# Performance work log

Hardware: AMD Instinct MI355X
Metric: run time of the kernel (lower is better)

The kernel has to match this reference:

```python
import jax, jax.numpy as jnp
from jax import lax
import numpy as np

KSIZE = 3      # match-patch size
STRIDE = 1
RATE = 2       # down/up-sampling rate
FUSE_K = 3
SCALE = 10.0   # softmax scale
DN = ('NHWC', 'HWIO', 'NHWC')


def extract_patches(x, k, s):
    """tf.image.extract_patches(..., padding='SAME'); returns [B, L, k, k, C]."""
    B, H, W, C = x.shape
    oh, ow = -(-H // s), -(-W // s)
    ph = max((oh - 1) * s + k - H, 0)
    pw = max((ow - 1) * s + k - W, 0)
    xp = jnp.pad(x, ((0, 0), (ph // 2, ph - ph // 2), (pw // 2, pw - pw // 2), (0, 0)))
    cols = [xp[:, i:i + oh * s:s, j:j + ow * s:s, :] for i in range(k) for j in range(k)]
    p = jnp.stack(cols, axis=3)                 # [B, oh, ow, k*k, C]
    return p.reshape(B, oh * ow, k, k, C)


def setup_inputs() -> dict:
    key = jax.random.key(0)
    k1, k2, k3 = jax.random.split(key, 3)
    B, H, W, C = 4, 96, 96, 64
    f = jax.random.normal(k1, (B, H, W, C), jnp.float32)
    b = jax.random.normal(k2, (B, H, W, C), jnp.float32)
    mask = jnp.zeros((B, H, W, 1), jnp.float32)          # 0 = no hole -> all patches valid
    fuse_weight = jax.random.normal(k3, (FUSE_K, FUSE_K, 1, 1), jnp.float32) * 0.3
    return {"f": f, "b": b, "mask": mask, "fuse_weight": fuse_weight}


def reference(f, b, mask, fuse_weight):
    B, H, W, C = f.shape
    kernel = 2 * RATE
    # deconv kernels from full-res background: [B, 4, 4, C, L]
    raw_w = extract_patches(b, kernel, RATE * STRIDE).transpose(0, 2, 3, 4, 1)
    fd = f[:, 1::2, 1::2, :]
    bd = b[:, 1::2, 1::2, :]
    md = mask[:, 1::2, 1::2, :]
    h, w_ = fd.shape[1], fd.shape[2]
    L = h * w_
    # matching kernels from downscaled background: [B, 3, 3, C, L]
    wk = extract_patches(bd, KSIZE, STRIDE).transpose(0, 2, 3, 4, 1)
    # mask patches -> per-patch validity mm: [B, L]
    mp = extract_patches(md, KSIZE, STRIDE)
    mm = (jnp.mean(mp, axis=(2, 3, 4)) == 0.0).astype(f.dtype)

    def per_sample(xi, wi, rwi, mmi):
        # xi: [h, w, C]; wi: [3,3,C,L]; rwi: [4,4,C,L]; mmi: [L]
        norm = jnp.maximum(jnp.sqrt(jnp.sum(wi * wi, axis=(0, 1, 2))), 1e-4)
        yi = lax.conv_general_dilated(xi[None], wi / norm, (1, 1), 'SAME',
                                      dimension_numbers=DN)[0]        # [h, w, L]
        # fuse: 3x3 conv over flattened [HW, HW] score map, twice (transposed view)
        y = yi.reshape(1, L, L, 1)
        y = lax.conv_general_dilated(y, fuse_weight, (1, 1), 'SAME', dimension_numbers=DN)
        y = y.reshape(h, w_, h, w_).transpose(1, 0, 3, 2).reshape(1, L, L, 1)
        y = lax.conv_general_dilated(y, fuse_weight, (1, 1), 'SAME', dimension_numbers=DN)
        y = y.reshape(w_, h, w_, h).transpose(1, 0, 3, 2).reshape(h, w_, L)
        # mask-gated scaled softmax over background patches
        y = y * mmi
        y = jax.nn.softmax(y * SCALE, axis=-1) * mmi
        # deconv-style combine with raw 4x4 patches, stride=rate
        out = lax.conv_transpose(y[None], rwi, (RATE, RATE), 'SAME',
                                 dimension_numbers=DN, transpose_kernel=True)[0] / 4.0
        return out                                                    # [H, W, C]

    return jax.vmap(per_sample)(fd, wk, raw_w, mm)
```

## Files before the change

### kernel.cpp

```cpp
#include <hip/hip_runtime.h>
#include <hip/hip_bf16.h>

#define KL  2304
#define KC  64
#define KHS 48
#define KHH 96
#define OFFY (KHS*(KL + 1))

typedef __attribute__((ext_vector_type(8))) short bf16x8;
typedef __attribute__((ext_vector_type(4))) short bf16x4;
typedef __attribute__((ext_vector_type(8))) _Float16 f16x8;
typedef __attribute__((ext_vector_type(4))) _Float16 f16x4;
typedef __attribute__((ext_vector_type(4))) float f32x4;

static __device__ inline unsigned short f2bf(float x) {
    __hip_bfloat16 h = __float2bfloat16(x);
    return *reinterpret_cast<unsigned short*>(&h);
}
static __device__ inline float bf2f(unsigned short u) {
    unsigned v = ((unsigned)u) << 16;
    return __uint_as_float(v);
}
static __device__ inline unsigned short f2h(float x) {
    _Float16 h = (_Float16)x;
    return *reinterpret_cast<unsigned short*>(&h);
}
static __device__ inline float h2f(unsigned short u) {
    _Float16 h = *reinterpret_cast<_Float16*>(&u);
    return (float)h;
}

__global__ __launch_bounds__(256) void k_prep2(const float* __restrict__ f,
    const float* __restrict__ bsrc, const float* __restrict__ mask,
    float* __restrict__ nbuf, float* __restrict__ mdd,
    unsigned short* __restrict__ Ahat, unsigned short* __restrict__ Bhat)
{
    int pp = blockIdx.x*4 + (threadIdx.x >> 6);
    int c = threadIdx.x & 63;
    int p = pp % KL, bi = pp / KL;
    int y = p / KHS, x = p % KHS;
    int fy = 2*y + 1;
    unsigned short* Ap = Ahat + ((size_t)bi*KL + p)*192;
    unsigned short* Bp = Bhat + ((size_t)bi*KL + p)*192;
    float bc = 0.f;
    #pragma unroll
    for (int dxi = 0; dxi < 3; dxi++) {
        int xx = x + dxi - 1;
        float av = 0.f, bv = 0.f;
        if ((unsigned)xx < KHS) {
            int fxx = 2*xx + 1;
            size_t src = (((size_t)bi*KHH + fy)*KHH + fxx)*KC + c;
            av = f[src]; bv = bsrc[src];
        }
        if (dxi == 1) bc = bv;
        Ap[dxi*64 + c] = f2h(av);
        Bp[dxi*64 + c] = f2h(bv);
    }
    float s = bc*bc;
    #pragma unroll
    for (int off = 32; off > 0; off >>= 1) s += __shfl_down(s, off);
    if (c == 0) {
        nbuf[bi*KL + p] = s;
        mdd[bi*KL + p]  = mask[((size_t)bi*KHH + fy)*KHH + (2*x + 1)];
    }
}

__global__ __launch_bounds__(256) void k_normmask(const float* __restrict__ nbuf,
    const float* __restrict__ mdd, float* __restrict__ rnrm, float* __restrict__ mm)
{
    int i = blockIdx.x*256 + threadIdx.x;
    int q = i % KL, bi = i / KL;
    int v = q / KHS, u = q % KHS;
    float sn = 0.f, sm = 0.f;
    for (int dy = -1; dy <= 1; dy++) {
        int vv = v + dy; if ((unsigned)vv >= KHS) continue;
        for (int dx = -1; dx <= 1; dx++) {
            int uu = u + dx; if ((unsigned)uu >= KHS) continue;
            sn += nbuf[bi*KL + vv*KHS + uu];
            sm += mdd[bi*KL + vv*KHS + uu];
        }
    }
    rnrm[i] = 1.0f / fmaxf(sqrtf(sn), 1e-4f);
    mm[i]   = (sm == 0.0f) ? 1.0f : 0.0f;
}

template<int KITERS, int OUTMODE, bool INFP16>
__global__ __launch_bounds__(256) void k_mfma_bt(const unsigned short* __restrict__ A,
    const unsigned short* __restrict__ B, void* __restrict__ Cv,
    int Ncols, size_t sA, size_t sB, size_t sC, int KDIM, int nsplit, size_t psize)
{
    int flat = blockIdx.x + gridDim.x*(blockIdx.y + gridDim.y*blockIdx.z);
    int nxy = gridDim.x*gridDim.y;
    int per = (nxy*gridDim.z) >> 3;
    int g = (flat & 7)*per + (flat >> 3);
    int z = g / nxy; int r = g - z*nxy;
    int by = r / gridDim.x; int bx = r - by*gridDim.x;

    int ks = z % nsplit, bi = z / nsplit;
    int kbase = ks * KITERS * 32;
    int n0 = bx*128, m0 = by*128;
    const unsigned short* Ab = A + (size_t)bi*sA;
    const unsigned short* Bb = B + (size_t)bi*sB;
    __shared__ unsigned short As[128*32];
    __shared__ unsigned short Bs[128*32];
    int t = threadIdx.x;
    int lane = t & 63, w = t >> 6;
    int l15 = lane & 15, quad = lane >> 4;
    int swf = (l15 >> 2) & 3;
    int wm = (w >> 1)*64, wn = (w & 1)*64;
    int srow = lane >> 2;
    int ch = lane & 3;
    f32x4 acc[4][4];
    #pragma unroll
    for (int i = 0; i < 4; i++)
        #pragma unroll
        for (int j = 0; j < 4; j++) acc[i][j] = (f32x4){0.f,0.f,0.f,0.f};

    for (int kk = 0; kk < KITERS; kk++) {
        int k0 = kbase + kk*32;
        #pragma unroll
        for (int i = 0; i < 2; i++) {
            int rbase = w*32 + i*16;
            int r2 = rbase + srow;
            int cs = (ch ^ ((r2 >> 2) & 3))*8;
            const unsigned short* ga = &Ab[(size_t)(m0 + r2)*KDIM + k0 + cs];
            __builtin_amdgcn_global_load_lds(
                (const __attribute__((address_space(1))) void*)ga,
                (__attribute__((address_space(3))) void*)&As[rbase*32], 16, 0, 0);
            const unsigned short* gb = &Bb[(size_t)(n0 + r2)*KDIM + k0 + cs];
            __builtin_amdgcn_global_load_lds(
                (const __attribute__((address_space(1))) void*)gb,
                (__attribute__((address_space(3))) void*)&Bs[rbase*32], 16, 0, 0);
        }
        __syncthreads();
        if (INFP16) {
            f16x8 af[4], bfr[4];
            #pragma unroll
            for (int mi = 0; mi < 4; mi++)
                af[mi] = *(const f16x8*)&As[(wm + mi*16 + l15)*32 + ((quad ^ swf)*8)];
            #pragma unroll
            for (int ni = 0; ni < 4; ni++)
                bfr[ni] = *(const f16x8*)&Bs[(wn + ni*16 + l15)*32 + ((quad ^ swf)*8)];
            #pragma unroll
            for (int mi = 0; mi < 4; mi++)
                #pragma unroll
                for (int ni = 0; ni < 4; ni++)
                    acc[mi][ni] = __builtin_amdgcn_mfma_f32_16x16x32_f16(
                        af[mi], bfr[ni], acc[mi][ni], 0, 0, 0);
        } else {
            bf16x8 af[4], bfr[4];
            #pragma unroll
            for (int mi = 0; mi < 4; mi++)
                af[mi] = *(const bf16x8*)&As[(wm + mi*16 + l15)*32 + ((quad ^ swf)*8)];
            #pragma unroll
            for (int ni = 0; ni < 4; ni++)
                bfr[ni] = *(const bf16x8*)&Bs[(wn + ni*16 + l15)*32 + ((quad ^ swf)*8)];
            #pragma unroll
            for (int mi = 0; mi < 4; mi++)
                #pragma unroll
                for (int ni = 0; ni < 4; ni++)
                    acc[mi][ni] = __builtin_amdgcn_mfma_f32_16x16x32_bf16(
                        af[mi], bfr[ni], acc[mi][ni], 0, 0, 0);
        }
        __syncthreads();
    }
    if (OUTMODE == 1 || OUTMODE == 2) {
        unsigned short* Cb = (unsigned short*)Cv + (size_t)ks*psize + (size_t)bi*sC;
        #pragma unroll
        for (int mi = 0; mi < 4; mi++)
            #pragma unroll
            for (int ni = 0; ni < 4; ni++) {
                int col = n0 + wn + ni*16 + l15;
                #pragma unroll
                for (int r2 = 0; r2 < 4; r2++) {
                    int row = m0 + wm + mi*16 + quad*4 + r2;
                    Cb[(size_t)row*Ncols + col] = (OUTMODE == 1)
                        ? f2bf(acc[mi][ni][r2]) : f2h(acc[mi][ni][r2]);
                }
            }
    } else {
        float* Cb = (float*)Cv + (size_t)ks*psize + (size_t)bi*sC;
        #pragma unroll
        for (int mi = 0; mi < 4; mi++)
            #pragma unroll
            for (int ni = 0; ni < 4; ni++) {
                int col = n0 + wn + ni*16 + l15;
                #pragma unroll
                for (int r2 = 0; r2 < 4; r2++) {
                    int row = m0 + wm + mi*16 + quad*4 + r2;
                    Cb[(size_t)row*Ncols + col] = acc[mi][ni][r2];
                }
            }
    }
}

#define KP_NT 24
#define STGA4(tt, j) do {                                                      \
    __builtin_amdgcn_global_load_lds(                                          \
        (const __attribute__((address_space(1))) void*)(gA + (size_t)(j)*128*2304 + (size_t)(tt)*32), \
        (__attribute__((address_space(3))) void*)&Atile[(tt)&3][((j)*128 + (w<<4))*32], 16, 0, 0); \
} while (0)
#define STGB4(tt, j) do {                                                      \
    __builtin_amdgcn_global_load_lds(                                          \
        (const __attribute__((address_space(1))) void*)(gB + (size_t)(j)*128*2304 + (size_t)(tt)*32), \
        (__attribute__((address_space(3))) void*)&Btile[(tt)&3][((j)*128 + (w<<4))*32], 16, 0, 0); \
} while (0)

#define MFMA_B(a, b, c) __builtin_amdgcn_mfma_f32_16x16x32_bf16(a, b, c, 0, 0, 0)

#define KT_BODY(kt, BVU, BVF) do {                                             \
    const unsigned short* At = &Atile[(kt) & 3][0];                            \
                                                          \
    __builtin_amdgcn_s_barrier();                                              \
    _Pragma("unroll")                                                          \
    for (int i = 0; i < 4; i++)                                                \
        af1[i] = *(const bf16x8*)&At[aOff + 2048 + i*512];                     \
    if ((kt) + 3 < KP_NT) { STGA4((kt)+3, 0); STGA4((kt)+3, 1); }              \
    __builtin_amdgcn_s_setprio(1);                                             \
    _Pragma("unroll")                                                          \
    for (int mi = 0; mi < 4; mi++)                                             \
        _Pragma("unroll")                                                      \
        for (int ni = 0; ni < 4; ni++)                                         \
            acc[mi][ni] = MFMA_B(af0[mi], BVU[ni], acc[mi][ni]);               \
    __builtin_amdgcn_s_setprio(0);                                             \
                                                          \
    __builtin_amdgcn_s_barrier();                                              \
    if ((kt) < KP_NT-1) {                                                      \
        if ((kt) <= KP_NT-4)      asm volatile("s_waitcnt vmcnt(6)" ::: "memory"); \
        else if ((kt) == KP_NT-3) asm volatile("s_waitcnt vmcnt(4)" ::: "memory"); \
        else                      asm volatile("s_waitcnt vmcnt(0)" ::: "memory"); \
        __builtin_amdgcn_sched_barrier(0);                                     \
        const unsigned short* An = &Atile[((kt)+1) & 3][0];                    \
        const unsigned short* Bn = &Btile[((kt)+1) & 3][0];                    \
        _Pragma("unroll")                                                      \
        for (int i = 0; i < 4; i++)                                            \
            af0[i] = *(const bf16x8*)&An[aOff + i*512];                        \
        _Pragma("unroll")                                                      \
        for (int ni = 0; ni < 4; ni++)                                         \
            BVF[ni] = *(const bf16x8*)&Bn[bOff + ni*512];                      \
    }                                                                          \
    if ((kt) + 3 < KP_NT) { STGB4((kt)+3, 0); STGB4((kt)+3, 1); }              \
    __builtin_amdgcn_s_setprio(1);                                             \
    _Pragma("unroll")                                                          \
    for (int mi = 0; mi < 4; mi++)                                             \
        _Pragma("unroll")                                                      \
        for (int ni = 0; ni < 4; ni++)                                         \
            acc[4+mi][ni] = MFMA_B(af1[mi], BVU[ni], acc[4+mi][ni]);           \
    __builtin_amdgcn_s_setprio(0);                                             \
} while (0)

__global__ __launch_bounds__(512, 2) void k_p8(
    const unsigned short* __restrict__ A,
    const unsigned short* __restrict__ B,
    unsigned short* __restrict__ C,
    size_t psize)
{
    __shared__ unsigned short Atile[4][8192];
    __shared__ unsigned short Btile[4][8192];

    int flat = blockIdx.x + gridDim.x*(blockIdx.y + gridDim.y*blockIdx.z);
    int nwg = gridDim.x*gridDim.y*gridDim.z;
    int qq = nwg >> 3, rr8 = nwg & 7;
    int xcd = flat & 7, sub = flat >> 3;
    int g = (xcd < rr8 ? xcd*(qq+1) : rr8*(qq+1) + (xcd - rr8)*qq) + sub;
    int nxy = gridDim.x*gridDim.y;
    int z = g / nxy; int rg = g - z*nxy;
    int by = rg / gridDim.x; int bx = rg - by*gridDim.x;

    int ks = z % 3, bi = z / 3;
    int kbase = ks * 768;
    int m0 = by * 256, n0 = bx * 256;
    const unsigned short* Ab = A + (size_t)bi * (2304ull*2304);
    const unsigned short* Bb = B + (size_t)bi * (1024ull*2304);

    int t = threadIdx.x;
    int w = t >> 6, lane = t & 63;
    int wr = w >> 2, wc = w & 3;
    int l15 = lane & 15, quad = lane >> 4;

    int scol = ((t & 3) ^ ((t >> 3) & 3))*8;
    const unsigned short* gA = Ab + (size_t)(m0 + (t >> 2))*2304 + kbase + scol;
    const unsigned short* gB = Bb + (size_t)(n0 + (t >> 2))*2304 + kbase + scol;

    int csw = (quad ^ ((l15 >> 1) & 3))*8;
    int aOff = (wr*128 + l15)*32 + csw;
    int bOff = (wc*64  + l15)*32 + csw;

    f32x4 acc[8][4];
    #pragma unroll
    for (int mi = 0; mi < 8; mi++)
        #pragma unroll
        for (int ni = 0; ni < 4; ni++) acc[mi][ni] = (f32x4){0.f,0.f,0.f,0.f};

    #pragma unroll
    for (int tt = 0; tt < 3; tt++) {
        STGA4(tt, 0); STGA4(tt, 1);
        STGB4(tt, 0); STGB4(tt, 1);
    }
    asm volatile("s_waitcnt vmcnt(8)" ::: "memory");
    __builtin_amdgcn_s_barrier();

    bf16x8 af0[4], af1[4], bvA[4], bvB[4];
    #pragma unroll
    for (int i = 0; i < 4; i++)
        af0[i] = *(const bf16x8*)&Atile[0][aOff + i*512];
    #pragma unroll
    for (int ni = 0; ni < 4; ni++)
        bvA[ni] = *(const bf16x8*)&Btile[0][bOff + ni*512];

    #pragma unroll 1
    for (int ktp = 0; ktp < KP_NT/2; ktp++) {
        int kt0 = ktp*2;
        KT_BODY(kt0,     bvA, bvB);
        KT_BODY(kt0 + 1, bvB, bvA);
    }

    unsigned short* Cb = C + (size_t)ks*psize + (size_t)bi*(2304ull*1024);
    #pragma unroll
    for (int mi = 0; mi < 8; mi++)
        #pragma unroll
        for (int ni = 0; ni < 4; ni++) {
            int col = n0 + wc*64 + ni*16 + l15;
            int rowb = m0 + wr*128 + mi*16 + quad*4;
            #pragma unroll
            for (int r = 0; r < 4; r++)
                Cb[(size_t)(rowb + r)*1024 + col] = f2bf(acc[mi][ni][r]);
        }
}

__global__ __launch_bounds__(256) void k_fuse_a2(const unsigned short* __restrict__ T,
    const float* __restrict__ rnrm, const float* __restrict__ fw,
    unsigned short* __restrict__ Y1)
{
    __shared__ float Sl[10][280];
    int flat = blockIdx.x + 9*(blockIdx.y + 288*blockIdx.z);
    int nwg = 2592*gridDim.z;
    int cpx = nwg >> 3;
    int g = (flat & 7)*cpx + (flat >> 3);
    int bi = g / 2592; int rem = g - bi*2592;
    int by = rem / 9;  int qt = rem - by*9;

    int p0 = by*8, q0 = qt*256;
    const unsigned short* Tb = T + (size_t)bi*KL*KL;
    const float* rn = rnrm + bi*KL;
    int t = threadIdx.x;
    bool edge = (qt == 0) | (qt == 8);
    if (!edge) {
        for (int idx = t; idx < 10*34; idx += 256) {
            int r = idx / 34, j = idx - r*34;
            int pp = p0 - 1 + r;
            int qq0 = q0 - 8 + j*8;
            float s[8];
            #pragma unroll
            for (int k = 0; k < 8; k++) s[k] = 0.f;
            if ((unsigned)pp < KL) {
                size_t base = (size_t)pp*KL + qq0;
                bool bm = (pp >= KHS), bp = (pp < KL - KHS);
                size_t offm = bm ? (size_t)OFFY : 0;
                size_t offp = bp ? (size_t)OFFY : 0;
                float fm = bm ? 1.f : 0.f, fp2 = bp ? 1.f : 0.f;
                f16x8 v0 = *(const f16x8*)&Tb[base];
                f16x8 vm = *(const f16x8*)&Tb[base - offm];
                f16x8 vp = *(const f16x8*)&Tb[base + offp];
                #pragma unroll
                for (int k = 0; k < 8; k++)
                    s[k] = ((float)v0[k] + fm*(float)vm[k] + fp2*(float)vp[k]) * rn[qq0 + k];
            }
            #pragma unroll
            for (int k = 0; k < 8; k++) Sl[r][j*8 + k] = s[k];
        }
    } else {
        for (int idx = t; idx < 10*272; idx += 256) {
            int r = idx / 272, c = idx - r*272;
            int pp = p0 - 1 + r, qq = q0 - 8 + c;
            float s = 0.f;
            if ((unsigned)pp < KL && (unsigned)qq < KL) {
                size_t base = (size_t)pp*KL + qq;
                float acc = h2f(Tb[base]);
                if (pp >= KHS && qq >= KHS)         acc += h2f(Tb[base - OFFY]);
                if (pp < KL - KHS && qq < KL - KHS) acc += h2f(Tb[base + OFFY]);
                s = acc * rn[qq];
            }
            Sl[r][c] = s;
        }
    }
    __syncthreads();
    float w[9];
    #pragma unroll
    for (int i = 0; i < 9; i++) w[i] = fw[i];
    int q = q0 + t;
    float h0[10], h1[10], h2[10];
    #pragma unroll
    for (int r = 0; r < 10; r++) {
        float s0 = Sl[r][t+7], s1 = Sl[r][t+8], s2 = Sl[r][t+9];
        h0[r] = w[0]*s0 + w[1]*s1 + w[2]*s2;
        h1[r] = w[3]*s0 + w[4]*s1 + w[5]*s2;
        h2[r] = w[6]*s0 + w[7]*s1 + w[8]*s2;
    }
    #pragma unroll
    for (int rr = 0; rr < 8; rr++) {
        Y1[((size_t)bi*KL + p0 + rr)*KL + q] = f2h(h0[rr] + h1[rr+1] + h2[rr+2]);
    }
}

__global__ __launch_bounds__(256) void k_fuse_b(const unsigned short* __restrict__ Y1,
    const float* __restrict__ fw, const float* __restrict__ mm,
    unsigned short* __restrict__ Ybf)
{
    __shared__ float rowb[6][KL];
    int blk = blockIdx.x;
    int tp0 = (blk % 576)*4;
    int bi  = blk / 576;
    int t = threadIdx.x;
    const unsigned short* Yb = Y1 + (size_t)bi*KL*KL;
    for (int idx = t; idx < 6*(KL/8); idx += 256) {
        int a = idx / (KL/8), i = idx - a*(KL/8);
        int t2 = tp0 - 1 + a;
        if ((unsigned)t2 < KL) {
            int pr = (t2 % KHS)*KHS + t2/KHS;
            f16x8 v = *(const f16x8*)&Yb[(size_t)pr*KL + i*8];
            #pragma unroll
            for (int j = 0; j < 8; j++) rowb[a][i*8 + j] = (float)v[j];
        } else {
            #pragma unroll
            for (int j = 0; j < 8; j++) rowb[a][i*8 + j] = 0.f;
        }
    }
    float w9[9];
    #pragma unroll
    for (int i = 0; i < 9; i++) w9[i] = fw[i];
    __syncthreads();
    int w = t >> 6, lane = t & 63;
    int tp = tp0 + w;
    int x = tp / KHS, y = tp - x*KHS;
    int p = y*KHS + x;
    const float* mmb = mm + bi*KL;
    float vals[36];
    float lmax = -1e30f;
    #pragma unroll
    for (int i = 0; i < 36; i++) {
        int q = lane + i*64;
        int qm = (q >= KHS)      ? q - KHS : 2255 + q;
        int qp = (q <= KL-1-KHS) ? q + KHS : q - 2255;
        float fm = (q != 0)    ? 1.f : 0.f;
        float fp = (q != KL-1) ? 1.f : 0.f;
        float am = w9[0]*rowb[w][qm] + w9[3]*rowb[w+1][qm] + w9[6]*rowb[w+2][qm];
        float a0 = w9[1]*rowb[w][q]  + w9[4]*rowb[w+1][q]  + w9[7]*rowb[w+2][q];
        float ap = w9[2]*rowb[w][qp] + w9[5]*rowb[w+1][qp] + w9[8]*rowb[w+2][qp];
        float val = (fm*am + a0 + fp*ap) * mmb[q] * 10.0f;
        vals[i] = val;
        lmax = fmaxf(lmax, val);
    }
    #pragma unroll
    for (int off = 32; off > 0; off >>= 1) lmax = fmaxf(lmax, __shfl_down(lmax, off));
    lmax = __shfl(lmax, 0);
    float lsum = 0.f;
    #pragma unroll
    for (int i = 0; i < 36; i++) {
        float e = __expf(vals[i] - lmax);
        vals[i] = e;
        lsum += e;
    }
    #pragma unroll
    for (int off = 32; off > 0; off >>= 1) lsum += __shfl_down(lsum, off);
    lsum = __shfl(lsum, 0);
    float inv = 1.0f / lsum;
    unsigned short* orow = Ybf + ((size_t)bi*KL + p)*KL;
    #pragma unroll
    for (int i = 0; i < 36; i++) {
        int q = lane + i*64;
        orow[q] = f2bf(vals[i]*inv*mmb[q]);
    }
}

__global__ __launch_bounds__(256) void k_buildRt(const float* __restrict__ bsrc,
    unsigned short* __restrict__ Rt)
{
    __shared__ unsigned short Ls[2][48][65];
    int blk = blockIdx.x;
    int vb = blk % 24;
    int jj = (blk / 24) % 16;
    int bi = blk / 384;
    int ky = jj >> 2, kx = jj & 3;
    int v0 = vb*2;
    int t = threadIdx.x;
    int c = t & 63, u4 = t >> 6;

    #pragma unroll
    for (int vv = 0; vv < 2; vv++) {
        int ry = 2*(v0 + vv) + ky - 1;
        bool ryok = (unsigned)ry < KHH;
        const float* brow = bsrc + (((size_t)bi*KHH + (ryok ? ry : 0))*KHH)*KC;
        #pragma unroll
        for (int j = 0; j < 12; j++) {
            int u = u4*12 + j;
            int rx = 2*u + kx - 1;
            float val = 0.f;
            if (ryok && (unsigned)rx < KHH)
                val = brow[(size_t)rx*KC + c];
            Ls[vv][u][c] = f2bf(val);
        }
    }
    __syncthreads();

    int cn = t >> 2, part = t & 3;
    unsigned short* orow = Rt + ((size_t)bi*1024 + jj*64 + cn)*KL + vb*96;
    #pragma unroll
    for (int ch = 0; ch < 3; ch++) {
        int ql = part*24 + ch*8;
        int vv = ql / 48;
        int ub = ql - vv*48;
        bf16x8 v8;
        #pragma unroll
        for (int j = 0; j < 8; j++)
            v8[j] = (short)Ls[vv][ub + j][cn];
        *(bf16x8*)&orow[ql] = v8;
    }
}

__global__ __launch_bounds__(256) void k_overlap(const unsigned short* __restrict__ P,
    float* __restrict__ out, size_t psize)
{
    size_t gid = (size_t)blockIdx.x*256 + threadIdx.x;
    int c8 = (int)(gid & 7)*8;
    size_t r = gid >> 3;
    int ix = (int)(r % KHH); r /= KHH;
    int iy = (int)(r % KHH);
    int bi = (int)(r / KHH);
    float acc[8];
    #pragma unroll
    for (int j = 0; j < 8; j++) acc[j] = 0.f;
    #pragma unroll
    for (int sy = 0; sy < 2; sy++) {
        int ky = (iy & 1) ? (sy*2) : (sy*2 + 1);
        int yp = (iy + 1 - ky) >> 1;
        if ((unsigned)yp >= KHS) continue;
        #pragma unroll
        for (int sx = 0; sx < 2; sx++) {
            int kx = (ix & 1) ? (sx*2) : (sx*2 + 1);
            int xp = (ix + 1 - kx) >> 1;
            if ((unsigned)xp >= KHS) continue;
            size_t idx = (((size_t)bi*KL + yp*KHS + xp)*16 + (ky*4 + kx))*64 + c8;
            #pragma unroll
            for (int s = 0; s < 3; s++) {
                bf16x8 v = *(const bf16x8*)&P[idx + s*psize];
                #pragma unroll
                for (int j = 0; j < 8; j++)
                    acc[j] += bf2f((unsigned short)v[j]);
            }
        }
    }
    float* op = &out[(((size_t)bi*KHH + iy)*KHH + ix)*KC + c8];
    f32x4 o0 = (f32x4){acc[0], acc[1], acc[2], acc[3]} * 0.25f;
    f32x4 o1 = (f32x4){acc[4], acc[5], acc[6], acc[7]} * 0.25f;
    *(f32x4*)&op[0] = o0;
    *(f32x4*)&op[4] = o1;
}

extern "C" void kernel_launch(void* const* d_in, const int* in_sizes, int n_in,
                              void* d_out, int out_size, void* d_ws, size_t ws_size,
                              hipStream_t stream)
{
    const float* f    = (const float*)d_in[0];
    const float* b    = (const float*)d_in[1];
    const float* mask = (const float*)d_in[2];
    const float* fw   = (const float*)d_in[3];
    float* out = (float*)d_out;

    auto need = [](int nbc) -> size_t {
        return (size_t)nbc * (2ull*KL*KC + 4ull*KL + 2ull*(size_t)KL*KL) * 4ull;
    };
    int nbc = 4;
    if (need(nbc) > ws_size) nbc = 2;
    if (need(nbc) > ws_size) nbc = 1;

    for (int bi0 = 0; bi0 < 4; bi0 += nbc) {
        int nb = (4 - bi0 < nbc) ? (4 - bi0) : nbc;
        const float* fc = f    + (size_t)bi0*KHH*KHH*KC;
        const float* bc = b    + (size_t)bi0*KHH*KHH*KC;
        const float* mc = mask + (size_t)bi0*KHH*KHH;
        float* outc = out + (size_t)bi0*KHH*KHH*KC;

        float* w    = (float*)d_ws;
        float* nbuf = w;  w += (size_t)nbc*KL;
        float* mdd  = w;  w += (size_t)nbc*KL;
        float* rnrm = w;  w += (size_t)nbc*KL;
        float* mmb  = w;  w += (size_t)nbc*KL;
        float* bufA = w;  w += (size_t)nbc*KL*KL;
        float* bufB = w;
        unsigned short* Ahat = (unsigned short*)bufB;
        unsigned short* Bhat = Ahat + (size_t)nbc*KL*192;
        unsigned short* Tbuf = (unsigned short*)bufA;
        unsigned short* Y1   = (unsigned short*)bufB;
        unsigned short* Ybf = (unsigned short*)bufA;
        unsigned short* Rtb = Ybf + (size_t)nbc*KL*KL;
        unsigned short* Pbuf = (unsigned short*)bufB;
        size_t psize = (size_t)nbc*KL*1024;

        k_prep2     <<<nb*KL/4, 256, 0, stream>>>(fc, bc, mc, nbuf, mdd, Ahat, Bhat);
        k_normmask  <<<(nb*KL)/256, 256, 0, stream>>>(nbuf, mdd, rnrm, mmb);
        k_mfma_bt<6,2,true><<<dim3(18, 18, nb), 256, 0, stream>>>(
            Ahat, Bhat, Tbuf, KL, (size_t)KL*192, (size_t)KL*192, (size_t)KL*KL,
            192, 1, 0);
        k_fuse_a2   <<<dim3(9, 288, nb), 256, 0, stream>>>(Tbuf, rnrm, fw, Y1);
        k_fuse_b    <<<nb*576, 256, 0, stream>>>(Y1, fw, mmb, Ybf);
        k_buildRt   <<<nb*384, 256, 0, stream>>>(bc, Rtb);
        k_p8<<<dim3(4, 9, nb*3), 512, 0, stream>>>(Ybf, Rtb, Pbuf, psize);
        k_overlap   <<<nb*288, 256, 0, stream>>>(Pbuf, outc, psize);
    }
}
```

Baseline: 242.5 us.

## Replace generic score GEMM with 256x256-tile pipelined fp16 MFMA kernel

The first matching GEMM (patch features times background patches, K=192) moves from the generic 128x128 single-buffered kernel to a dedicated 512-thread kernel with 256x256 tiles. It uses a 4-stage LDS ring with asynchronous global-to-LDS loads issued three tiles ahead, explicit vmcnt waits, raw barriers and setprio around the MFMA bursts. The aim is to overlap loads with MFMA work and increase reuse per tile. The costs are higher LDS and register use per block, and a smaller grid (324 blocks) that may leave some CUs idle.

```diff
diff --git a/kernel.cpp b/kernel.cpp
--- a/kernel.cpp
+++ b/kernel.cpp
@@ -84,114 +84,135 @@
     mm[i]   = (sm == 0.0f) ? 1.0f : 0.0f;
 }
 
-template<int KITERS, int OUTMODE, bool INFP16>
-__global__ __launch_bounds__(256) void k_mfma_bt(const unsigned short* __restrict__ A,
-    const unsigned short* __restrict__ B, void* __restrict__ Cv,
-    int Ncols, size_t sA, size_t sB, size_t sC, int KDIM, int nsplit, size_t psize)
-{
+#define TP_NT 6
+#define T_STGA(tt, j) do {                                                     \
+    __builtin_amdgcn_global_load_lds(                                          \
+        (const __attribute__((address_space(1))) void*)(gA + (size_t)(j)*128*192 + (size_t)(tt)*32), \
+        (__attribute__((address_space(3))) void*)&Atile[(tt)&3][((j)*128 + (w<<4))*32], 16, 0, 0); \
+} while (0)
+#define T_STGB(tt, j) do {                                                     \
+    __builtin_amdgcn_global_load_lds(                                          \
+        (const __attribute__((address_space(1))) void*)(gB + (size_t)(j)*128*192 + (size_t)(tt)*32), \
+        (__attribute__((address_space(3))) void*)&Btile[(tt)&3][((j)*128 + (w<<4))*32], 16, 0, 0); \
+} while (0)
+
+#define MFMA_H(a, b, c) __builtin_amdgcn_mfma_f32_16x16x32_f16(a, b, c, 0, 0, 0)
+
+#define KT_BODY_T(kt, BVU, BVF) do {                                           \
+    const unsigned short* At = &Atile[(kt) & 3][0];                            \
+                                                          \
+    __builtin_amdgcn_s_barrier();                                              \
+    _Pragma("unroll")                                                          \
+    for (int i = 0; i < 4; i++)                                                \
+        af1[i] = *(const f16x8*)&At[aOff + 2048 + i*512];                      \
+    if ((kt) + 3 < TP_NT) { T_STGA((kt)+3, 0); T_STGA((kt)+3, 1); }            \
+    __builtin_amdgcn_s_setprio(1);                                             \
+    _Pragma("unroll")                                                          \
+    for (int mi = 0; mi < 4; mi++)                                             \
+        _Pragma("unroll")                                                      \
+        for (int ni = 0; ni < 4; ni++)                                         \
+            acc[mi][ni] = MFMA_H(af0[mi], BVU[ni], acc[mi][ni]);               \
+    __builtin_amdgcn_s_setprio(0);                                             \
+                                                          \
+    __builtin_amdgcn_s_barrier();                                              \
+    if ((kt) < TP_NT-1) {                                                      \
+        if ((kt) <= TP_NT-4)      asm volatile("s_waitcnt vmcnt(6)" ::: "memory"); \
+        else if ((kt) == TP_NT-3) asm volatile("s_waitcnt vmcnt(4)" ::: "memory"); \
+        else                      asm volatile("s_waitcnt vmcnt(0)" ::: "memory"); \
+        __builtin_amdgcn_sched_barrier(0);                                     \
+        const unsigned short* An = &Atile[((kt)+1) & 3][0];                    \
+        const unsigned short* Bn = &Btile[((kt)+1) & 3][0];                    \
+        _Pragma("unroll")                                                      \
+        for (int i = 0; i < 4; i++)                                            \
+            af0[i] = *(const f16x8*)&An[aOff + i*512];                         \
+        _Pragma("unroll")                                                      \
+        for (int ni = 0; ni < 4; ni++)                                         \
+            BVF[ni] = *(const f16x8*)&Bn[bOff + ni*512];                       \
+    }                                                                          \
+    if ((kt) + 3 < TP_NT) { T_STGB((kt)+3, 0); T_STGB((kt)+3, 1); }            \
+    __builtin_amdgcn_s_setprio(1);                                             \
+    _Pragma("unroll")                                                          \
+    for (int mi = 0; mi < 4; mi++)                                             \
+        _Pragma("unroll")                                                      \
+        for (int ni = 0; ni < 4; ni++)                                         \
+            acc[4+mi][ni] = MFMA_H(af1[mi], BVU[ni], acc[4+mi][ni]);           \
+    __builtin_amdgcn_s_setprio(0);                                             \
+} while (0)
+
+__global__ __launch_bounds__(512, 2) void k_t8(
+    const unsigned short* __restrict__ A,
+    const unsigned short* __restrict__ B,
+    unsigned short* __restrict__ T)
+{
+    __shared__ unsigned short Atile[4][8192];
+    __shared__ unsigned short Btile[4][8192];
+
     int flat = blockIdx.x + gridDim.x*(blockIdx.y + gridDim.y*blockIdx.z);
+    int nwg = gridDim.x*gridDim.y*gridDim.z;
+    int qq = nwg >> 3, rr8 = nwg & 7;
+    int xcd = flat & 7, sub = flat >> 3;
+    int g = (xcd < rr8 ? xcd*(qq+1) : rr8*(qq+1) + (xcd - rr8)*qq) + sub;
     int nxy = gridDim.x*gridDim.y;
-    int per = (nxy*gridDim.z) >> 3;
-    int g = (flat & 7)*per + (flat >> 3);
-    int z = g / nxy; int r = g - z*nxy;
-    int by = r / gridDim.x; int bx = r - by*gridDim.x;
-
-    int ks = z % nsplit, bi = z / nsplit;
-    int kbase = ks * KITERS * 32;
-    int n0 = bx*128, m0 = by*128;
-    const unsigned short* Ab = A + (size_t)bi*sA;
-    const unsigned short* Bb = B + (size_t)bi*sB;
-    __shared__ unsigned short As[128*32];
-    __shared__ unsigned short Bs[128*32];
+    int bi = g / nxy; int rg = g - bi*nxy;
+    int by = rg / gridDim.x; int bx = rg - by*gridDim.x;
+
+    int m0 = by * 256, n0 = bx * 256;
+    const unsigned short* Ab = A + (size_t)bi * ((size_t)KL*192);
+    const unsigned short* Bb = B + (size_t)bi * ((size_t)KL*192);
+
     int t = threadIdx.x;
-    int lane = t & 63, w = t >> 6;
+    int w = t >> 6, lane = t & 63;
+    int wr = w >> 2, wc = w & 3;
     int l15 = lane & 15, quad = lane >> 4;
-    int swf = (l15 >> 2) & 3;
-    int wm = (w >> 1)*64, wn = (w & 1)*64;
-    int srow = lane >> 2;
-    int ch = lane & 3;
-    f32x4 acc[4][4];
+
+    int scol = ((t & 3) ^ ((t >> 3) & 3))*8;
+    const unsigned short* gA = Ab + (size_t)(m0 + (t >> 2))*192 + scol;
+    const unsigned short* gB = Bb + (size_t)(n0 + (t >> 2))*192 + scol;
+
+    int csw = (quad ^ ((l15 >> 1) & 3))*8;
+    int aOff = (wr*128 + l15)*32 + csw;
+    int bOff = (wc*64  + l15)*32 + csw;
+
+    f32x4 acc[8][4];
+    #pragma unroll
+    for (int mi = 0; mi < 8; mi++)
+        #pragma unroll
+        for (int ni = 0; ni < 4; ni++) acc[mi][ni] = (f32x4){0.f,0.f,0.f,0.f};
+
+    #pragma unroll
+    for (int tt = 0; tt < 3; tt++) {
+        T_STGA(tt, 0); T_STGA(tt, 1);
+        T_STGB(tt, 0); T_STGB(tt, 1);
+    }
+    asm volatile("s_waitcnt vmcnt(8)" ::: "memory");
+    __builtin_amdgcn_s_barrier();
+
+    f16x8 af0[4], af1[4], bvA[4], bvB[4];
     #pragma unroll
     for (int i = 0; i < 4; i++)
+        af0[i] = *(const f16x8*)&Atile[0][aOff + i*512];
+    #pragma unroll
+    for (int ni = 0; ni < 4; ni++)
+        bvA[ni] = *(const f16x8*)&Btile[0][bOff + ni*512];
+
+    #pragma unroll 1
+    for (int ktp = 0; ktp < TP_NT/2; ktp++) {
+        int kt0 = ktp*2;
+        KT_BODY_T(kt0,     bvA, bvB);
+        KT_BODY_T(kt0 + 1, bvB, bvA);
+    }
+
+    unsigned short* Tb = T + (size_t)bi*((size_t)KL*KL);
+    #pragma unroll
+    for (int mi = 0; mi < 8; mi++)
         #pragma unroll
-        for (int j = 0; j < 4; j++) acc[i][j] = (f32x4){0.f,0.f,0.f,0.f};
-
-    for (int kk = 0; kk < KITERS; kk++) {
-        int k0 = kbase + kk*32;
-        #pragma unroll
-        for (int i = 0; i < 2; i++) {
-            int rbase = w*32 + i*16;
-            int r2 = rbase + srow;
-            int cs = (ch ^ ((r2 >> 2) & 3))*8;
-            const unsigned short* ga = &Ab[(size_t)(m0 + r2)*KDIM + k0 + cs];
-            __builtin_amdgcn_global_load_lds(
-                (const __attribute__((address_space(1))) void*)ga,
-                (__attribute__((address_space(3))) void*)&As[rbase*32], 16, 0, 0);
-            const unsigned short* gb = &Bb[(size_t)(n0 + r2)*KDIM + k0 + cs];
-            __builtin_amdgcn_global_load_lds(
-                (const __attribute__((address_space(1))) void*)gb,
-                (__attribute__((address_space(3))) void*)&Bs[rbase*32], 16, 0, 0);
-        }
-        __syncthreads();
-        if (INFP16) {
-            f16x8 af[4], bfr[4];
+        for (int ni = 0; ni < 4; ni++) {
+            int col = n0 + wc*64 + ni*16 + l15;
+            int rowb = m0 + wr*128 + mi*16 + quad*4;
             #pragma unroll
-            for (int mi = 0; mi < 4; mi++)
-                af[mi] = *(const f16x8*)&As[(wm + mi*16 + l15)*32 + ((quad ^ swf)*8)];
-            #pragma unroll
-            for (int ni = 0; ni < 4; ni++)
-                bfr[ni] = *(const f16x8*)&Bs[(wn + ni*16 + l15)*32 + ((quad ^ swf)*8)];
-            #pragma unroll
-            for (int mi = 0; mi < 4; mi++)
-                #pragma unroll
-                for (int ni = 0; ni < 4; ni++)
-                    acc[mi][ni] = __builtin_amdgcn_mfma_f32_16x16x32_f16(
-                        af[mi], bfr[ni], acc[mi][ni], 0, 0, 0);
-        } else {
-            bf16x8 af[4], bfr[4];
-            #pragma unroll
-            for (int mi = 0; mi < 4; mi++)
-                af[mi] = *(const bf16x8*)&As[(wm + mi*16 + l15)*32 + ((quad ^ swf)*8)];
-            #pragma unroll
-            for (int ni = 0; ni < 4; ni++)
-                bfr[ni] = *(const bf16x8*)&Bs[(wn + ni*16 + l15)*32 + ((quad ^ swf)*8)];
-            #pragma unroll
-            for (int mi = 0; mi < 4; mi++)
-                #pragma unroll
-                for (int ni = 0; ni < 4; ni++)
-                    acc[mi][ni] = __builtin_amdgcn_mfma_f32_16x16x32_bf16(
-                        af[mi], bfr[ni], acc[mi][ni], 0, 0, 0);
-        }
-        __syncthreads();
-    }
-    if (OUTMODE == 1 || OUTMODE == 2) {
-        unsigned short* Cb = (unsigned short*)Cv + (size_t)ks*psize + (size_t)bi*sC;
-        #pragma unroll
-        for (int mi = 0; mi < 4; mi++)
-            #pragma unroll
-            for (int ni = 0; ni < 4; ni++) {
-                int col = n0 + wn + ni*16 + l15;
-                #pragma unroll
-                for (int r2 = 0; r2 < 4; r2++) {
-                    int row = m0 + wm + mi*16 + quad*4 + r2;
-                    Cb[(size_t)row*Ncols + col] = (OUTMODE == 1)
-                        ? f2bf(acc[mi][ni][r2]) : f2h(acc[mi][ni][r2]);
-                }
-            }
-    } else {
-        float* Cb = (float*)Cv + (size_t)ks*psize + (size_t)bi*sC;
-        #pragma unroll
-        for (int mi = 0; mi < 4; mi++)
-            #pragma unroll
-            for (int ni = 0; ni < 4; ni++) {
-                int col = n0 + wn + ni*16 + l15;
-                #pragma unroll
-                for (int r2 = 0; r2 < 4; r2++) {
-                    int row = m0 + wm + mi*16 + quad*4 + r2;
-                    Cb[(size_t)row*Ncols + col] = acc[mi][ni][r2];
-                }
-            }
-    }
+            for (int r = 0; r < 4; r++)
+                Tb[(size_t)(rowb + r)*KL + col] = f2h(acc[mi][ni][r]);
+        }
 }
 
 #define KP_NT 24
@@ -599,9 +620,7 @@
 
         k_prep2     <<<nb*KL/4, 256, 0, stream>>>(fc, bc, mc, nbuf, mdd, Ahat, Bhat);
         k_normmask  <<<(nb*KL)/256, 256, 0, stream>>>(nbuf, mdd, rnrm, mmb);
-        k_mfma_bt<6,2,true><<<dim3(18, 18, nb), 256, 0, stream>>>(
-            Ahat, Bhat, Tbuf, KL, (size_t)KL*192, (size_t)KL*192, (size_t)KL*KL,
-            192, 1, 0);
+        k_t8<<<dim3(9, 9, nb), 512, 0, stream>>>(Ahat, Bhat, Tbuf);
         k_fuse_a2   <<<dim3(9, 288, nb), 256, 0, stream>>>(Tbuf, rnrm, fw, Y1);
         k_fuse_b    <<<nb*576, 256, 0, stream>>>(Y1, fw, mmb, Ybf);
         k_buildRt   <<<nb*384, 256, 0, stream>>>(bc, Rtb);
```

Measured after the change: 247.7 us (median of 2 runs). +2.1%, slower.
